# Optimization experiments

Measured on AMD Instinct MI355X. Metric: run time of the kernel, lower is better.

## Reference

```python
import jax, jax.numpy as jnp
import numpy as np

N, E, D = 100000, 640000, 128


def _xavier(key, shape):
    return jax.random.normal(key, shape, jnp.float32) * np.float32(np.sqrt(2.0 / (shape[0] + shape[1])))


def setup_inputs() -> dict:
    key = jax.random.key(0)
    ks = jax.random.split(key, 16)
    inp = {
        "x": jax.random.normal(ks[0], (N, D), jnp.float32),
        "prompt_h": jax.random.normal(ks[1], (N, D), jnp.float32),
        "edge_attr": jax.random.normal(ks[2], (E, D), jnp.float32),
        "prompt_e": jax.random.normal(ks[3], (E, D), jnp.float32),
        "edge_index": jax.random.randint(ks[4], (2, E), 0, N, dtype=jnp.int32),
        # Linear weights stored [in, out] (torch stores [out, in]; math identical)
        "Wq": _xavier(ks[5], (D, D)), "bq": jnp.zeros((D,), jnp.float32),
        "Wk": _xavier(ks[6], (D, D)), "bk": jnp.zeros((D,), jnp.float32),
        "Wv": _xavier(ks[7], (D, D)), "bv": jnp.zeros((D,), jnp.float32),
        "We1": _xavier(ks[8], (D, D)), "be1": jnp.zeros((D,), jnp.float32),
        "We2": _xavier(ks[9], (D, D)), "be2": jnp.zeros((D,), jnp.float32),
        "Wh": _xavier(ks[10], (D, D)), "bh": jnp.zeros((D,), jnp.float32),
        "Wf1": _xavier(ks[11], (D, 2 * D)), "bf1": jnp.zeros((2 * D,), jnp.float32),
        "Wf2": _xavier(ks[12], (2 * D, D)), "bf2": jnp.zeros((D,), jnp.float32),
    }
    return inp


def reference(x, prompt_h, edge_attr, prompt_e, edge_index,
              Wq, bq, Wk, bk, Wv, bv, We1, be1, We2, be2,
              Wh, bh, Wf1, bf1, Wf2, bf2):
    relu = jax.nn.relu
    # Projections (dropout=0, eval mode)
    Q = x @ Wq + bq                      # [N, D]
    K = prompt_h @ Wk + bk               # [N, D]
    V = prompt_h @ Wv + bv               # [N, D]
    h = relu(Q * K)                      # attn_product='mul', score_act with relu
    # Edge-enhanced messages: gather source node scores per edge
    src = h[edge_index[0]]               # [E, D]
    e = relu((edge_attr + prompt_e) @ We1 + be1)
    e = relu((e + prompt_e) @ We2 + be2)  # updated edge_attr (update_e=True)
    msg = relu(src + e)                  # [E, D]
    # scatter-add aggregation into destination nodes
    aggr = jax.ops.segment_sum(msg, edge_index[1], num_segments=x.shape[0])  # [N, D]
    h_out = relu((h + V + aggr) @ Wh + bh)
    h_out = h_out + x                    # residual (in_dim == out_dim)
    h_out = relu(h_out @ Wf1 + bf1)
    h_out = h_out @ Wf2 + bf2            # [N, D]
    return h_out, e
```

## Files before the change

kernel.cpp:

```cpp
#include <hip/hip_runtime.h>

typedef __attribute__((ext_vector_type(8))) short bfrag;
typedef __attribute__((ext_vector_type(4))) float f4;

__device__ __forceinline__ unsigned short f2b(float f) {
  unsigned int u = __builtin_bit_cast(unsigned int, f);
  u = (u + 0x7fffu + ((u >> 16) & 1u)) >> 16;
  return (unsigned short)u;
}
__device__ __forceinline__ float b2f(unsigned short s) {
  unsigned int u = ((unsigned int)s) << 16;
  return __builtin_bit_cast(float, u);
}
__device__ __forceinline__ float relu(float v) { return v > 0.f ? v : 0.f; }

template <bool ADD>
__device__ __forceinline__ void stage_A(char* dst, const float* s0, const float* s1,
                                        long r0, long maxRow) {
  const int tid = threadIdx.x;
#pragma unroll
  for (int i = 0; i < 4; ++i) {
    int ch = tid + (i << 8);
    int row = ch >> 4, kg = ch & 15;
    long gr = r0 + row;
    float v[8];
    if (gr < maxRow) {
      const float4* p = (const float4*)(s0 + gr * 128 + kg * 8);
      float4 a = p[0], b = p[1];
      v[0] = a.x; v[1] = a.y; v[2] = a.z; v[3] = a.w;
      v[4] = b.x; v[5] = b.y; v[6] = b.z; v[7] = b.w;
      if (ADD) {
        const float4* q = (const float4*)(s1 + gr * 128 + kg * 8);
        float4 c = q[0], d = q[1];
        v[0] += c.x; v[1] += c.y; v[2] += c.z; v[3] += c.w;
        v[4] += d.x; v[5] += d.y; v[6] += d.z; v[7] += d.w;
      }
    } else {
#pragma unroll
      for (int j = 0; j < 8; ++j) v[j] = 0.f;
    }
    union { unsigned short h[8]; uint4 u; } pk;
#pragma unroll
    for (int j = 0; j < 8; ++j) pk.h[j] = f2b(v[j]);
    *(uint4*)(dst + (((row << 8) + (kg << 4)) ^ ((row & 7) << 4))) = pk.u;
  }
}

__device__ __forceinline__ void stage_W(char* dst, const unsigned short* src,
                                        int rowStride, int kOff) {
  const int tid = threadIdx.x;
#pragma unroll
  for (int i = 0; i < 8; ++i) {
    int ch = tid + (i << 8);
    int col = ch >> 4, kg = ch & 15;
    uint4 u = *(const uint4*)(src + (size_t)col * rowStride + kOff + kg * 8);
    *(uint4*)(dst + (((col << 8) + (kg << 4)) ^ ((col & 7) << 4))) = u;
  }
}

__device__ __forceinline__ void stage_Wh(char* dst, const unsigned short* src,
                                         int rowStride, int kOff) {
  const int tid = threadIdx.x;
#pragma unroll
  for (int i = 0; i < 4; ++i) {
    int ch = tid + (i << 8);
    int c = ch >> 3, kg = ch & 7;
    uint4 u = *(const uint4*)(src + (size_t)c * rowStride + kOff + kg * 8);
    *(uint4*)(dst + (((c << 7) + (kg << 4)) ^ ((c & 7) << 4))) = u;
  }
}

__device__ __forceinline__ void mm(const char* A, const char* W, int wm, int wn,
                                   int lane, f4 acc[2][4]) {
#pragma unroll
  for (int kk = 0; kk < 4; ++kk) {
    bfrag a[2], b[4];
#pragma unroll
    for (int rt = 0; rt < 2; ++rt) {
      int row = (wm << 5) + (rt << 4) + (lane & 15);
      a[rt] = *(const bfrag*)(A + (((row << 8) + (kk << 6) + ((lane >> 4) << 4)) ^ ((row & 7) << 4)));
    }
#pragma unroll
    for (int ct = 0; ct < 4; ++ct) {
      int col = (wn << 6) + (ct << 4) + (lane & 15);
      b[ct] = *(const bfrag*)(W + (((col << 8) + (kk << 6) + ((lane >> 4) << 4)) ^ ((col & 7) << 4)));
    }
#pragma unroll
    for (int rt = 0; rt < 2; ++rt)
#pragma unroll
      for (int ct = 0; ct < 4; ++ct)
        acc[rt][ct] = __builtin_amdgcn_mfma_f32_16x16x32_bf16(a[rt], b[ct], acc[rt][ct], 0, 0, 0);
  }
}

__device__ __forceinline__ void mm_h(const char* A, const char* W, int wm, int wn,
                                     int lane, f4 acc[2][4], int kh) {
#pragma unroll
  for (int kk2 = 0; kk2 < 2; ++kk2) {
    int kA = (kh << 1) + kk2;
    bfrag a[2], b[4];
#pragma unroll
    for (int rt = 0; rt < 2; ++rt) {
      int row = (wm << 5) + (rt << 4) + (lane & 15);
      a[rt] = *(const bfrag*)(A + (((row << 8) + (kA << 6) + ((lane >> 4) << 4)) ^ ((row & 7) << 4)));
    }
#pragma unroll
    for (int ct = 0; ct < 4; ++ct) {
      int col = (wn << 6) + (ct << 4) + (lane & 15);
      b[ct] = *(const bfrag*)(W + (((col << 7) + (kk2 << 6) + ((lane >> 4) << 4)) ^ ((col & 7) << 4)));
    }
#pragma unroll
    for (int rt = 0; rt < 2; ++rt)
#pragma unroll
      for (int ct = 0; ct < 4; ++ct)
        acc[rt][ct] = __builtin_amdgcn_mfma_f32_16x16x32_bf16(a[rt], b[ct], acc[rt][ct], 0, 0, 0);
  }
}

__global__ void k_prep(const float* __restrict__ Wq, const float* __restrict__ Wk,
                       const float* __restrict__ Wv, const float* __restrict__ We1,
                       const float* __restrict__ We2, const float* __restrict__ Wh,
                       const float* __restrict__ Wf1, const float* __restrict__ Wf2,
                       unsigned short* __restrict__ wt) {
  int b = blockIdx.x, t = threadIdx.x;
  if (b < 384) {
    int m = b >> 6;
    const float* tbl[6] = {Wq, Wk, Wv, We1, We2, Wh};
    const float* src = tbl[m];
    int local = ((b & 63) << 8) + t;
    int n = local >> 7, k = local & 127;
    wt[m * 16384 + local] = f2b(src[k * 128 + n]);
  } else if (b < 512) {
    int local = ((b - 384) << 8) + t;
    int n = local >> 7, k = local & 127;
    wt[98304 + local] = f2b(Wf1[k * 256 + n]);
  } else {
    int local = ((b - 512) << 8) + t;
    int n = local >> 8, k = local & 255;
    wt[131072 + local] = f2b(Wf2[k * 128 + n]);
  }
}

__global__ void k_deg(const int* __restrict__ ei, int* __restrict__ deg, long E) {
  long g = (long)blockIdx.x * 256 + threadIdx.x;
  if (g < E) atomicAdd(deg + ei[E + g], 1);
}

__global__ void k_scanA(const int* __restrict__ deg, int* __restrict__ ex,
                        int* __restrict__ bsum, int n) {
  __shared__ int s[256];
  int t = threadIdx.x; int g = blockIdx.x * 256 + t;
  int v = (g < n) ? deg[g] : 0;
  int val = v;
  s[t] = val; __syncthreads();
#pragma unroll
  for (int o = 1; o < 256; o <<= 1) {
    int u = (t >= o) ? s[t - o] : 0;
    __syncthreads();
    val += u; s[t] = val;
    __syncthreads();
  }
  if (g < n) ex[g] = val - v;
  if (t == 255) bsum[blockIdx.x] = val;
}

__global__ void k_scanB(int* __restrict__ bsum, int nb) {
  __shared__ int s[1024];
  int t = threadIdx.x;
  int v = (t < nb) ? bsum[t] : 0;
  int val = v;
  s[t] = val; __syncthreads();
#pragma unroll
  for (int o = 1; o < 1024; o <<= 1) {
    int u = (t >= o) ? s[t - o] : 0;
    __syncthreads();
    val += u; s[t] = val;
    __syncthreads();
  }
  if (t < nb) bsum[t] = val - v;
}

__global__ void k_scanC(const int* __restrict__ ex, const int* __restrict__ bsum,
                        int* __restrict__ off, int* __restrict__ cursor, int n) {
  int g = blockIdx.x * 256 + threadIdx.x;
  if (g < n) {
    int o = ex[g] + bsum[blockIdx.x];
    off[g] = o; cursor[g] = o;
  }
}

__global__ void k_fill(const int* __restrict__ ei, int* __restrict__ cursor,
                       int* __restrict__ eidx, long E) {
  long g = (long)blockIdx.x * 256 + threadIdx.x;
  if (g < E) {
    int pos = atomicAdd(cursor + ei[E + g], 1);
    eidx[pos] = (int)g;
  }
}

__global__ __launch_bounds__(256, 2) void k_nodes1(
    const float* __restrict__ x, const float* __restrict__ ph,
    const float* __restrict__ bq, const float* __restrict__ bk,
    const float* __restrict__ bv, const unsigned short* __restrict__ wt,
    unsigned short* __restrict__ hbf, float* __restrict__ hpv, long N) {
  extern __shared__ char sm[];
  char* Ax = sm;
  char* Aph = sm + 16384;
  char* Wl = sm + 32768;
  long n0 = (long)blockIdx.x * 64;
  stage_A<false>(Ax, x, nullptr, n0, N);
  stage_A<false>(Aph, ph, nullptr, n0, N);
  stage_W(Wl, wt + 0, 128, 0);
  __syncthreads();
  const int tid = threadIdx.x, lane = tid & 63, w = tid >> 6, wm = w >> 1, wn = w & 1;
  f4 accQ[2][4] = {};
  mm(Ax, Wl, wm, wn, lane, accQ);
  __syncthreads();
  stage_W(Wl, wt + 16384, 128, 0);
  __syncthreads();
  f4 accK[2][4] = {};
  mm(Aph, Wl, wm, wn, lane, accK);
  __syncthreads();
  stage_W(Wl, wt + 32768, 128, 0);
  __syncthreads();
  f4 accV[2][4] = {};
  mm(Aph, Wl, wm, wn, lane, accV);
#pragma unroll
  for (int ct = 0; ct < 4; ++ct) {
    int col = (wn << 6) + (ct << 4) + (lane & 15);
    float vbq = bq[col], vbk = bk[col], vbv = bv[col];
#pragma unroll
    for (int rt = 0; rt < 2; ++rt)
#pragma unroll
      for (int j = 0; j < 4; ++j) {
        int rl = (wm << 5) + (rt << 4) + ((lane >> 4) << 2) + j;
        long row = n0 + rl;
        if (row < N) {
          float q = accQ[rt][ct][j] + vbq;
          float k = accK[rt][ct][j] + vbk;
          float v = accV[rt][ct][j] + vbv;
          float h = relu(q * k);
          hbf[row * 128 + col] = f2b(h);
          hpv[row * 128 + col] = h + v;
        }
      }
  }
}

__global__ __launch_bounds__(256, 3) void k_edges(
    const float* __restrict__ ea, const float* __restrict__ pe,
    const float* __restrict__ be1, const float* __restrict__ be2,
    const unsigned short* __restrict__ wt, const int* __restrict__ ei,
    const unsigned short* __restrict__ hbf, unsigned short* __restrict__ msg,
    float* __restrict__ eout, long E) {
  extern __shared__ char sm[];
  char* A = sm;
  unsigned short* peL = (unsigned short*)(sm + 16384);
  char* Wl = sm + 32768;
  char* stg = sm + 16384;
  int* srcI = (int*)(sm + 49152);
  const int tid = threadIdx.x;
  long e0 = (long)blockIdx.x * 64;
  if (tid < 64) srcI[tid] = (e0 + tid < E) ? ei[e0 + tid] : 0;
#pragma unroll
  for (int i = 0; i < 4; ++i) {
    int ch = tid + (i << 8);
    int row = ch >> 4, kg = ch & 15;
    long gr = e0 + row;
    union { unsigned short h[8]; uint4 u; } s, q;
    if (gr < E) {
      const float4* pa = (const float4*)(ea + gr * 128 + kg * 8);
      const float4* pp = (const float4*)(pe + gr * 128 + kg * 8);
      float4 a0 = pa[0], a1 = pa[1];
      float4 p0 = pp[0], p1 = pp[1];
      s.h[0] = f2b(a0.x + p0.x); s.h[1] = f2b(a0.y + p0.y);
      s.h[2] = f2b(a0.z + p0.z); s.h[3] = f2b(a0.w + p0.w);
      s.h[4] = f2b(a1.x + p1.x); s.h[5] = f2b(a1.y + p1.y);
      s.h[6] = f2b(a1.z + p1.z); s.h[7] = f2b(a1.w + p1.w);
      q.h[0] = f2b(p0.x); q.h[1] = f2b(p0.y); q.h[2] = f2b(p0.z); q.h[3] = f2b(p0.w);
      q.h[4] = f2b(p1.x); q.h[5] = f2b(p1.y); q.h[6] = f2b(p1.z); q.h[7] = f2b(p1.w);
    } else {
      s.u = uint4{0, 0, 0, 0}; q.u = uint4{0, 0, 0, 0};
    }
    *(uint4*)((char*)peL + (row << 8) + (kg << 4)) = q.u;
    *(uint4*)(A + (((row << 8) + (kg << 4)) ^ ((row & 7) << 4))) = s.u;
  }
  stage_Wh(Wl, wt + 49152, 128, 0);
  __syncthreads();
  const int lane = tid & 63, w = tid >> 6, wm = w >> 1, wn = w & 1;
  f4 acc[2][4] = {};
  mm_h(A, Wl, wm, wn, lane, acc, 0);
  __syncthreads();
  stage_Wh(Wl, wt + 49152, 128, 64);
  __syncthreads();
  mm_h(A, Wl, wm, wn, lane, acc, 1);
  __syncthreads();
  const int c0 = (tid & 31) << 2;
  const float4 vb1 = *(const float4*)(be1 + c0);
#pragma unroll
  for (int h = 0; h < 2; ++h) {
    if (wm == h) {
#pragma unroll
      for (int ct = 0; ct < 4; ++ct) {
        int col = (wn << 6) + (ct << 4) + (lane & 15);
#pragma unroll
        for (int rt = 0; rt < 2; ++rt)
#pragma unroll
          for (int j = 0; j < 4; ++j) {
            int lr = (rt << 4) + ((lane >> 4) << 2) + j;
            *(float*)(Wl + (((lr << 9) + (col << 2)) ^ ((lr & 7) << 4))) = acc[rt][ct][j];
          }
      }
    }
    __syncthreads();
#pragma unroll
    for (int it = 0; it < 4; ++it) {
      int lr = (tid >> 5) + (it << 3);
      int r = (h << 5) + lr;
      f4 a = *(const f4*)(Wl + (((lr << 9) + (c0 << 2)) ^ ((lr & 7) << 4)));
      uint2 pu = *(const uint2*)(peL + (r << 7) + c0);
      float p0 = b2f((unsigned short)pu.x), p1 = b2f((unsigned short)(pu.x >> 16));
      float p2 = b2f((unsigned short)pu.y), p3 = b2f((unsigned short)(pu.y >> 16));
      unsigned short t0 = f2b(relu(a[0] + vb1.x) + p0);
      unsigned short t1 = f2b(relu(a[1] + vb1.y) + p1);
      unsigned short t2 = f2b(relu(a[2] + vb1.z) + p2);
      unsigned short t3 = f2b(relu(a[3] + vb1.w) + p3);
      uint2 op;
      op.x = (unsigned int)t0 | ((unsigned int)t1 << 16);
      op.y = (unsigned int)t2 | ((unsigned int)t3 << 16);
      *(uint2*)(A + (((r << 8) + (c0 << 1)) ^ ((r & 7) << 4))) = op;
    }
    __syncthreads();
  }
  stage_Wh(Wl, wt + 65536, 128, 0);
  __syncthreads();
  f4 acc2[2][4] = {};
  mm_h(A, Wl, wm, wn, lane, acc2, 0);
  __syncthreads();
  stage_Wh(Wl, wt + 65536, 128, 64);
  __syncthreads();
  mm_h(A, Wl, wm, wn, lane, acc2, 1);
  __syncthreads();
#pragma unroll
  for (int ct = 0; ct < 4; ++ct) {
    int col = (wn << 6) + (ct << 4) + (lane & 15);
#pragma unroll
    for (int rt = 0; rt < 2; ++rt)
#pragma unroll
      for (int j = 0; j < 4; ++j) {
        int rl = (wm << 5) + (rt << 4) + ((lane >> 4) << 2) + j;
        *(float*)(stg + (((rl << 9) + (col << 2)) ^ ((rl & 7) << 4))) = acc2[rt][ct][j];
      }
  }
  __syncthreads();
  const float4 vb2 = *(const float4*)(be2 + c0);
#pragma unroll
  for (int it = 0; it < 8; ++it) {
    int r = (tid >> 5) + (it << 3);
    long edge = e0 + r;
    if (edge < E) {
      f4 a = *(const f4*)(stg + (((r << 9) + (c0 << 2)) ^ ((r & 7) << 4)));
      float ev0 = relu(a[0] + vb2.x), ev1 = relu(a[1] + vb2.y);
      float ev2 = relu(a[2] + vb2.z), ev3 = relu(a[3] + vb2.w);
      float4 ov; ov.x = ev0; ov.y = ev1; ov.z = ev2; ov.w = ev3;
      *(float4*)(eout + edge * 128 + c0) = ov;
      uint2 hu = *(const uint2*)(hbf + (long)srcI[r] * 128 + c0);
      float h0 = b2f((unsigned short)hu.x), h1 = b2f((unsigned short)(hu.x >> 16));
      float h2 = b2f((unsigned short)hu.y), h3 = b2f((unsigned short)(hu.y >> 16));
      unsigned short m0 = f2b(relu(ev0 + h0)), m1 = f2b(relu(ev1 + h1));
      unsigned short m2 = f2b(relu(ev2 + h2)), m3 = f2b(relu(ev3 + h3));
      uint2 mo;
      mo.x = (unsigned int)m0 | ((unsigned int)m1 << 16);
      mo.y = (unsigned int)m2 | ((unsigned int)m3 << 16);
      *(uint2*)(msg + edge * 128 + c0) = mo;
    }
  }
}

__global__ __launch_bounds__(256, 2) void k_edges_at(
    const float* __restrict__ ea, const float* __restrict__ pe,
    const float* __restrict__ be1, const float* __restrict__ be2,
    const unsigned short* __restrict__ wt, const int* __restrict__ ei,
    const unsigned short* __restrict__ hbf, float* __restrict__ aggr,
    float* __restrict__ eout, long E) {
  extern __shared__ char sm[];
  char* A = sm;
  unsigned short* peL = (unsigned short*)(sm + 16384);
  char* Wl = sm + 32768;
  int* srcI = (int*)(sm + 65536);
  int* dstI = srcI + 64;
  const int tid = threadIdx.x;
  long e0 = (long)blockIdx.x * 64;
  if (tid < 64) {
    long ge = e0 + tid;
    srcI[tid] = (ge < E) ? ei[ge] : 0;
    dstI[tid] = (ge < E) ? ei[E + ge] : 0;
  }
#pragma unroll
  for (int i = 0; i < 4; ++i) {
    int ch = tid + (i << 8);
    int row = ch >> 4, kg = ch & 15;
    long gr = e0 + row;
    union { unsigned short h[8]; uint4 u; } s, q;
    if (gr < E) {
      const float4* pa = (const float4*)(ea + gr * 128 + kg * 8);
      const float4* pp = (const float4*)(pe + gr * 128 + kg * 8);
      float4 a0 = pa[0], a1 = pa[1];
      float4 p0 = pp[0], p1 = pp[1];
      s.h[0] = f2b(a0.x + p0.x); s.h[1] = f2b(a0.y + p0.y);
      s.h[2] = f2b(a0.z + p0.z); s.h[3] = f2b(a0.w + p0.w);
      s.h[4] = f2b(a1.x + p1.x); s.h[5] = f2b(a1.y + p1.y);
      s.h[6] = f2b(a1.z + p1.z); s.h[7] = f2b(a1.w + p1.w);
      q.h[0] = f2b(p0.x); q.h[1] = f2b(p0.y); q.h[2] = f2b(p0.z); q.h[3] = f2b(p0.w);
      q.h[4] = f2b(p1.x); q.h[5] = f2b(p1.y); q.h[6] = f2b(p1.z); q.h[7] = f2b(p1.w);
    } else {
      s.u = uint4{0, 0, 0, 0}; q.u = uint4{0, 0, 0, 0};
    }
    *(uint4*)((char*)peL + (row << 8) + (kg << 4)) = q.u;
    *(uint4*)(A + (((row << 8) + (kg << 4)) ^ ((row & 7) << 4))) = s.u;
  }
  stage_W(Wl, wt + 49152, 128, 0);
  __syncthreads();
  const int lane = tid & 63, w = tid >> 6, wm = w >> 1, wn = w & 1;
  f4 acc[2][4] = {};
  mm(A, Wl, wm, wn, lane, acc);
  __syncthreads();
#pragma unroll
  for (int ct = 0; ct < 4; ++ct) {
    int col = (wn << 6) + (ct << 4) + (lane & 15);
    float b1 = be1[col];
#pragma unroll
    for (int rt = 0; rt < 2; ++rt)
#pragma unroll
      for (int j = 0; j < 4; ++j) {
        int rl = (wm << 5) + (rt << 4) + ((lane >> 4) << 2) + j;
        float tv = relu(acc[rt][ct][j] + b1) + b2f(peL[rl * 128 + col]);
        *(unsigned short*)(A + (((rl << 8) + (col << 1)) ^ ((rl & 7) << 4))) = f2b(tv);
      }
  }
  stage_W(Wl, wt + 65536, 128, 0);
  __syncthreads();
  f4 acc2[2][4] = {};
  mm(A, Wl, wm, wn, lane, acc2);
#pragma unroll
  for (int ct = 0; ct < 4; ++ct) {
    int col = (wn << 6) + (ct << 4) + (lane & 15);
    float b2 = be2[col];
#pragma unroll
    for (int rt = 0; rt < 2; ++rt)
#pragma unroll
      for (int j = 0; j < 4; ++j) {
        int rl = (wm << 5) + (rt << 4) + ((lane >> 4) << 2) + j;
        long edge = e0 + rl;
        if (edge < E) {
          float ev = relu(acc2[rt][ct][j] + b2);
          eout[edge * 128 + col] = ev;
          float hs = b2f(hbf[(long)srcI[rl] * 128 + col]);
          float m = relu(ev + hs);
          atomicAdd(aggr + (long)dstI[rl] * 128 + col, m);
        }
      }
  }
}

__global__ __launch_bounds__(256) void k_aggr(
    const int* __restrict__ off, const int* __restrict__ deg,
    const int* __restrict__ eidx, const unsigned short* __restrict__ msg,
    float* __restrict__ aggr, long N) {
  long node = (long)blockIdx.x * 4 + (threadIdx.x >> 6);
  if (node >= N) return;
  const int lane = threadIdx.x & 63;
  int st = off[node], d = deg[node];
  float a0 = 0.f, a1 = 0.f;
  for (int i = 0; i < d; ++i) {
    int eid = eidx[st + i];
    unsigned int u = *(const unsigned int*)(msg + (long)eid * 128 + lane * 2);
    a0 += b2f((unsigned short)u);
    a1 += b2f((unsigned short)(u >> 16));
  }
  *(float2*)(aggr + node * 128 + lane * 2) = float2{a0, a1};
}

__global__ __launch_bounds__(256, 2) void k_nodes2(
    const float* __restrict__ hpv, const float* __restrict__ aggr,
    const float* __restrict__ x, const float* __restrict__ bh,
    const float* __restrict__ bf1, const float* __restrict__ bf2,
    const unsigned short* __restrict__ wt, float* __restrict__ out, long N) {
  extern __shared__ char sm[];
  char* A = sm;
  char* T = sm + 16384;
  char* Wl = sm + 32768;
  long n0 = (long)blockIdx.x * 64;
  const int tid = threadIdx.x;
  stage_A<true>(A, hpv, aggr, n0, N);
  stage_W(Wl, wt + 81920, 128, 0);
  __syncthreads();
  const int lane = tid & 63, w = tid >> 6, wm = w >> 1, wn = w & 1;
  f4 acc1[2][4] = {};
  mm(A, Wl, wm, wn, lane, acc1);
  __syncthreads();
#pragma unroll
  for (int ct = 0; ct < 4; ++ct) {
    int col = (wn << 6) + (ct << 4) + (lane & 15);
    float bb = bh[col];
#pragma unroll
    for (int rt = 0; rt < 2; ++rt)
#pragma unroll
      for (int j = 0; j < 4; ++j) {
        int rl = (wm << 5) + (rt << 4) + ((lane >> 4) << 2) + j;
        long row = n0 + rl;
        float xv = (row < N) ? x[row * 128 + col] : 0.f;
        float tv = relu(acc1[rt][ct][j] + bb) + xv;
        *(unsigned short*)(T + (((rl << 8) + (col << 1)) ^ ((rl & 7) << 4))) = f2b(tv);
      }
  }
  stage_W(Wl, wt + 98304, 128, 0);
  __syncthreads();
  f4 accA[2][4] = {};
  mm(T, Wl, wm, wn, lane, accA);
  __syncthreads();
#pragma unroll
  for (int ct = 0; ct < 4; ++ct) {
    int col = (wn << 6) + (ct << 4) + (lane & 15);
    float bb = bf1[col];
#pragma unroll
    for (int rt = 0; rt < 2; ++rt)
#pragma unroll
      for (int j = 0; j < 4; ++j) {
        int rl = (wm << 5) + (rt << 4) + ((lane >> 4) << 2) + j;
        float uv = relu(accA[rt][ct][j] + bb);
        *(unsigned short*)(A + (((rl << 8) + (col << 1)) ^ ((rl & 7) << 4))) = f2b(uv);
      }
  }
  stage_W(Wl, wt + 131072, 256, 0);
  __syncthreads();
  f4 acc3[2][4] = {};
  mm(A, Wl, wm, wn, lane, acc3);
  __syncthreads();
  stage_W(Wl, wt + 114688, 128, 0);
  __syncthreads();
  f4 accB[2][4] = {};
  mm(T, Wl, wm, wn, lane, accB);
  __syncthreads();
#pragma unroll
  for (int ct = 0; ct < 4; ++ct) {
    int col = (wn << 6) + (ct << 4) + (lane & 15);
    float bb = bf1[128 + col];
#pragma unroll
    for (int rt = 0; rt < 2; ++rt)
#pragma unroll
      for (int j = 0; j < 4; ++j) {
        int rl = (wm << 5) + (rt << 4) + ((lane >> 4) << 2) + j;
        float uv = relu(accB[rt][ct][j] + bb);
        *(unsigned short*)(A + (((rl << 8) + (col << 1)) ^ ((rl & 7) << 4))) = f2b(uv);
      }
  }
  stage_W(Wl, wt + 131072, 256, 128);
  __syncthreads();
  mm(A, Wl, wm, wn, lane, acc3);
#pragma unroll
  for (int ct = 0; ct < 4; ++ct) {
    int col = (wn << 6) + (ct << 4) + (lane & 15);
    float bb = bf2[col];
#pragma unroll
    for (int rt = 0; rt < 2; ++rt)
#pragma unroll
      for (int j = 0; j < 4; ++j) {
        int rl = (wm << 5) + (rt << 4) + ((lane >> 4) << 2) + j;
        long row = n0 + rl;
        if (row < N) out[row * 128 + col] = acc3[rt][ct][j] + bb;
      }
  }
}

extern "C" void kernel_launch(void* const* d_in, const int* in_sizes, int n_in,
                              void* d_out, int out_size, void* d_ws, size_t ws_size,
                              hipStream_t stream) {
  const float* x   = (const float*)d_in[0];
  const float* ph  = (const float*)d_in[1];
  const float* ea  = (const float*)d_in[2];
  const float* pe  = (const float*)d_in[3];
  const int*   ei  = (const int*)d_in[4];
  const float* Wq  = (const float*)d_in[5];  const float* bq  = (const float*)d_in[6];
  const float* Wk  = (const float*)d_in[7];  const float* bk  = (const float*)d_in[8];
  const float* Wv  = (const float*)d_in[9];  const float* bv  = (const float*)d_in[10];
  const float* We1 = (const float*)d_in[11]; const float* be1 = (const float*)d_in[12];
  const float* We2 = (const float*)d_in[13]; const float* be2 = (const float*)d_in[14];
  const float* Wh  = (const float*)d_in[15]; const float* bh  = (const float*)d_in[16];
  const float* Wf1 = (const float*)d_in[17]; const float* bf1 = (const float*)d_in[18];
  const float* Wf2 = (const float*)d_in[19]; const float* bf2 = (const float*)d_in[20];
  const long N = in_sizes[0] / 128;
  const long E = in_sizes[2] / 128;

  char* ws = (char*)d_ws;
  size_t pos = 0;
  auto alloc = [&](size_t bytes) { size_t p = pos; pos += (bytes + 255) & ~255ULL; return p; };
  size_t o_wt   = alloc(327680);
  size_t o_hbf  = alloc((size_t)N * 256);
  size_t o_hpv  = alloc((size_t)N * 512);
  size_t o_aggr = alloc((size_t)N * 512);
  size_t base_needed = pos;
  size_t o_deg  = alloc((size_t)N * 4);
  size_t o_ex   = alloc((size_t)N * 4);
  size_t o_cur  = alloc((size_t)N * 4);
  size_t o_off  = alloc((size_t)N * 4);
  size_t o_bsum = alloc(4096);
  size_t o_eidx = alloc((size_t)E * 4);
  size_t o_msg  = alloc((size_t)E * 256);
  size_t csr_needed = pos;
  (void)base_needed;

  unsigned short* wt  = (unsigned short*)(ws + o_wt);
  unsigned short* hbf = (unsigned short*)(ws + o_hbf);
  float* hpv  = (float*)(ws + o_hpv);
  float* aggr = (float*)(ws + o_aggr);
  float* outH = (float*)d_out;
  float* outE = outH + N * 128;

  k_prep<<<640, 256, 0, stream>>>(Wq, Wk, Wv, We1, We2, Wh, Wf1, Wf2, wt);
  int nb = (int)((N + 63) / 64);
  int eb = (int)((E + 63) / 64);
  k_nodes1<<<nb, 256, 65536, stream>>>(x, ph, bq, bk, bv, wt, hbf, hpv, N);

  if (ws_size >= csr_needed) {
    int* deg = (int*)(ws + o_deg);
    int* ex  = (int*)(ws + o_ex);
    int* cur = (int*)(ws + o_cur);
    int* off = (int*)(ws + o_off);
    int* bsum = (int*)(ws + o_bsum);
    int* eidx = (int*)(ws + o_eidx);
    unsigned short* msg = (unsigned short*)(ws + o_msg);
    int nb1 = (int)((N + 255) / 256);
    hipMemsetAsync(deg, 0, (size_t)N * 4, stream);
    k_deg<<<(int)((E + 255) / 256), 256, 0, stream>>>(ei, deg, E);
    k_scanA<<<nb1, 256, 0, stream>>>(deg, ex, bsum, (int)N);
    k_scanB<<<1, 1024, 0, stream>>>(bsum, nb1);
    k_scanC<<<nb1, 256, 0, stream>>>(ex, bsum, off, cur, (int)N);
    k_fill<<<(int)((E + 255) / 256), 256, 0, stream>>>(ei, cur, eidx, E);
    k_edges<<<eb, 256, 49408, stream>>>(ea, pe, be1, be2, wt, ei, hbf, msg, outE, E);
    k_aggr<<<(int)((N + 3) / 4), 256, 0, stream>>>(off, deg, eidx, msg, aggr, N);
  } else {
    hipMemsetAsync(aggr, 0, (size_t)N * 512, stream);
    k_edges_at<<<eb, 256, 66048, stream>>>(ea, pe, be1, be2, wt, ei, hbf, aggr, outE, E);
  }
  k_nodes2<<<nb, 256, 65536, stream>>>(hpv, aggr, x, bh, bf1, bf2, wt, outH, N);
}
```

Before: 624.4 us.

## Write messages in CSR order and fuse aggregation into node MLP kernel

k_fill now records each edge's destination slot, and k_edges writes its message directly at that CSR position, so aggregation reads contiguous rows instead of following an index array. The separate k_aggr kernel and the fp32 aggr buffer round trip are removed: k_nodes2 gathers its segment sums straight into its shared-memory A tile. Shared-memory footprints are cut (half-width weight staging, one A buffer, edge-side data held in registers) and launch bounds raised to fit more blocks per CU, and node outputs go out as coalesced row stores through an LDS staging tile. The risks are higher register pressure from the per-thread arrays and extra barriers from the split weight staging.

```diff
diff --git a/kernel.cpp b/kernel.cpp
--- a/kernel.cpp
+++ b/kernel.cpp
@@ -114,6 +114,60 @@
 #pragma unroll
       for (int ct = 0; ct < 4; ++ct)
         acc[rt][ct] = __builtin_amdgcn_mfma_f32_16x16x32_bf16(a[rt], b[ct], acc[rt][ct], 0, 0, 0);
+  }
+}
+
+__device__ __forceinline__ void dump_half(char* Wl, const f4 acc[2][4], int lane, int wn) {
+#pragma unroll
+  for (int ct = 0; ct < 4; ++ct) {
+    int col = (wn << 6) + (ct << 4) + (lane & 15);
+#pragma unroll
+    for (int rt = 0; rt < 2; ++rt)
+#pragma unroll
+      for (int j = 0; j < 4; ++j) {
+        int lr = (rt << 4) + ((lane >> 4) << 2) + j;
+        *(float*)(Wl + (((lr << 9) + (col << 2)) ^ ((lr & 7) << 4))) = acc[rt][ct][j];
+      }
+  }
+}
+
+__device__ __forceinline__ void dump_full(char* stg, const f4 acc[2][4], int lane, int wm, int wn) {
+#pragma unroll
+  for (int ct = 0; ct < 4; ++ct) {
+    int col = (wn << 6) + (ct << 4) + (lane & 15);
+#pragma unroll
+    for (int rt = 0; rt < 2; ++rt)
+#pragma unroll
+      for (int j = 0; j < 4; ++j) {
+        int rl = (wm << 5) + (rt << 4) + ((lane >> 4) << 2) + j;
+        *(float*)(stg + (((rl << 9) + (col << 2)) ^ ((rl & 7) << 4))) = acc[rt][ct][j];
+      }
+  }
+}
+
+template <bool ADDX>
+__device__ __forceinline__ void trans_half(const char* Wl, char* dstT, const float* xsrc,
+                                           float4 vb, long n0, long N,
+                                           int h, int team, int c0) {
+#pragma unroll
+  for (int it = 0; it < 4; ++it) {
+    int lr = team + (it << 3);
+    int r = (h << 5) + lr;
+    f4 a = *(const f4*)(Wl + (((lr << 9) + (c0 << 2)) ^ ((lr & 7) << 4)));
+    float x0 = 0.f, x1 = 0.f, x2 = 0.f, x3 = 0.f;
+    long row = n0 + r;
+    if (ADDX && row < N) {
+      float4 xv = *(const float4*)(xsrc + row * 128 + c0);
+      x0 = xv.x; x1 = xv.y; x2 = xv.z; x3 = xv.w;
+    }
+    float t0 = relu(a[0] + vb.x) + x0;
+    float t1 = relu(a[1] + vb.y) + x1;
+    float t2 = relu(a[2] + vb.z) + x2;
+    float t3 = relu(a[3] + vb.w) + x3;
+    uint2 op;
+    op.x = (unsigned)f2b(t0) | ((unsigned)f2b(t1) << 16);
+    op.y = (unsigned)f2b(t2) | ((unsigned)f2b(t3) << 16);
+    *(uint2*)(dstT + (((r << 8) + (c0 << 1)) ^ ((r & 7) << 4))) = op;
   }
 }
 
@@ -190,41 +244,39 @@
 }
 
 __global__ void k_fill(const int* __restrict__ ei, int* __restrict__ cursor,
-                       int* __restrict__ eidx, long E) {
+                       int* __restrict__ pos, long E) {
   long g = (long)blockIdx.x * 256 + threadIdx.x;
-  if (g < E) {
-    int pos = atomicAdd(cursor + ei[E + g], 1);
-    eidx[pos] = (int)g;
-  }
-}
-
-__global__ __launch_bounds__(256, 2) void k_nodes1(
+  if (g < E) pos[g] = atomicAdd(cursor + ei[E + g], 1);
+}
+
+__global__ __launch_bounds__(256, 3) void k_nodes1(
     const float* __restrict__ x, const float* __restrict__ ph,
     const float* __restrict__ bq, const float* __restrict__ bk,
     const float* __restrict__ bv, const unsigned short* __restrict__ wt,
     unsigned short* __restrict__ hbf, float* __restrict__ hpv, long N) {
   extern __shared__ char sm[];
-  char* Ax = sm;
-  char* Aph = sm + 16384;
-  char* Wl = sm + 32768;
+  char* A = sm;
+  char* Wl = sm + 16384;
   long n0 = (long)blockIdx.x * 64;
-  stage_A<false>(Ax, x, nullptr, n0, N);
-  stage_A<false>(Aph, ph, nullptr, n0, N);
+  const int tid = threadIdx.x, lane = tid & 63, w = tid >> 6, wm = w >> 1, wn = w & 1;
+  const int team = tid >> 5, c0 = (tid & 31) << 2;
+  stage_A<false>(A, x, nullptr, n0, N);
   stage_W(Wl, wt + 0, 128, 0);
   __syncthreads();
-  const int tid = threadIdx.x, lane = tid & 63, w = tid >> 6, wm = w >> 1, wn = w & 1;
   f4 accQ[2][4] = {};
-  mm(Ax, Wl, wm, wn, lane, accQ);
-  __syncthreads();
+  mm(A, Wl, wm, wn, lane, accQ);
+  __syncthreads();
+  stage_A<false>(A, ph, nullptr, n0, N);
   stage_W(Wl, wt + 16384, 128, 0);
   __syncthreads();
   f4 accK[2][4] = {};
-  mm(Aph, Wl, wm, wn, lane, accK);
+  mm(A, Wl, wm, wn, lane, accK);
   __syncthreads();
   stage_W(Wl, wt + 32768, 128, 0);
   __syncthreads();
   f4 accV[2][4] = {};
-  mm(Aph, Wl, wm, wn, lane, accV);
+  mm(A, Wl, wm, wn, lane, accV);
+  __syncthreads();
 #pragma unroll
   for (int ct = 0; ct < 4; ++ct) {
     int col = (wn << 6) + (ct << 4) + (lane & 15);
@@ -234,34 +286,149 @@
 #pragma unroll
       for (int j = 0; j < 4; ++j) {
         int rl = (wm << 5) + (rt << 4) + ((lane >> 4) << 2) + j;
-        long row = n0 + rl;
-        if (row < N) {
-          float q = accQ[rt][ct][j] + vbq;
-          float k = accK[rt][ct][j] + vbk;
-          float v = accV[rt][ct][j] + vbv;
-          float h = relu(q * k);
-          hbf[row * 128 + col] = f2b(h);
-          hpv[row * 128 + col] = h + v;
-        }
+        float q = accQ[rt][ct][j] + vbq;
+        float k = accK[rt][ct][j] + vbk;
+        float v = accV[rt][ct][j] + vbv;
+        float h = relu(q * k);
+        *(unsigned short*)(A + (((rl << 8) + (col << 1)) ^ ((rl & 7) << 4))) = f2b(h);
+        *(float*)(Wl + (((rl << 9) + (col << 2)) ^ ((rl & 7) << 4))) = h + v;
       }
   }
-}
-
-__global__ __launch_bounds__(256, 3) void k_edges(
+  __syncthreads();
+#pragma unroll
+  for (int it = 0; it < 8; ++it) {
+    int r = team + (it << 3);
+    long row = n0 + r;
+    if (row < N) {
+      uint2 hb = *(const uint2*)(A + (((r << 8) + (c0 << 1)) ^ ((r & 7) << 4)));
+      f4 hv = *(const f4*)(Wl + (((r << 9) + (c0 << 2)) ^ ((r & 7) << 4)));
+      *(uint2*)(hbf + row * 128 + c0) = hb;
+      float4 ov; ov.x = hv[0]; ov.y = hv[1]; ov.z = hv[2]; ov.w = hv[3];
+      *(float4*)(hpv + row * 128 + c0) = ov;
+    }
+  }
+}
+
+__global__ __launch_bounds__(256, 5) void k_edges(
     const float* __restrict__ ea, const float* __restrict__ pe,
     const float* __restrict__ be1, const float* __restrict__ be2,
     const unsigned short* __restrict__ wt, const int* __restrict__ ei,
-    const unsigned short* __restrict__ hbf, unsigned short* __restrict__ msg,
+    const int* __restrict__ pos, const unsigned short* __restrict__ hbf,
+    unsigned short* __restrict__ msg, float* __restrict__ eout, long E) {
+  extern __shared__ char sm[];
+  char* A = sm;
+  char* Wl = sm + 16384;
+  char* stg = sm;
+  const int tid = threadIdx.x;
+  const int team = tid >> 5, c0 = (tid & 31) << 2;
+  const int lane = tid & 63, w = tid >> 6, wm = w >> 1, wn = w & 1;
+  long e0 = (long)blockIdx.x * 64;
+
+  int srcR[8], posR[8];
+  uint2 peR[8];
+#pragma unroll
+  for (int it = 0; it < 8; ++it) {
+    int r = team + (it << 3);
+    long ge = e0 + r;
+    srcR[it] = (ge < E) ? ei[ge] : 0;
+    posR[it] = (ge < E) ? pos[ge] : 0;
+    float4 av = make_float4(0.f, 0.f, 0.f, 0.f), pv = av;
+    if (ge < E) {
+      av = *(const float4*)(ea + ge * 128 + c0);
+      pv = *(const float4*)(pe + ge * 128 + c0);
+    }
+    peR[it].x = (unsigned)f2b(pv.x) | ((unsigned)f2b(pv.y) << 16);
+    peR[it].y = (unsigned)f2b(pv.z) | ((unsigned)f2b(pv.w) << 16);
+    uint2 s;
+    s.x = (unsigned)f2b(av.x + pv.x) | ((unsigned)f2b(av.y + pv.y) << 16);
+    s.y = (unsigned)f2b(av.z + pv.z) | ((unsigned)f2b(av.w + pv.w) << 16);
+    *(uint2*)(A + (((r << 8) + (c0 << 1)) ^ ((r & 7) << 4))) = s;
+  }
+  stage_Wh(Wl, wt + 49152, 128, 0);
+  __syncthreads();
+  f4 acc[2][4] = {};
+  mm_h(A, Wl, wm, wn, lane, acc, 0);
+  __syncthreads();
+  stage_Wh(Wl, wt + 49152, 128, 64);
+  __syncthreads();
+  mm_h(A, Wl, wm, wn, lane, acc, 1);
+  __syncthreads();
+  const float4 vb1 = *(const float4*)(be1 + c0);
+#pragma unroll
+  for (int h = 0; h < 2; ++h) {
+    if (wm == h) dump_half(Wl, acc, lane, wn);
+    __syncthreads();
+#pragma unroll
+    for (int it = 0; it < 4; ++it) {
+      int lr = team + (it << 3);
+      int r = (h << 5) + lr;
+      int j = (h << 2) + it;
+      f4 a = *(const f4*)(Wl + (((lr << 9) + (c0 << 2)) ^ ((lr & 7) << 4)));
+      float p0 = b2f((unsigned short)peR[j].x), p1 = b2f((unsigned short)(peR[j].x >> 16));
+      float p2 = b2f((unsigned short)peR[j].y), p3 = b2f((unsigned short)(peR[j].y >> 16));
+      float t0 = relu(a[0] + vb1.x) + p0;
+      float t1 = relu(a[1] + vb1.y) + p1;
+      float t2 = relu(a[2] + vb1.z) + p2;
+      float t3 = relu(a[3] + vb1.w) + p3;
+      uint2 op;
+      op.x = (unsigned)f2b(t0) | ((unsigned)f2b(t1) << 16);
+      op.y = (unsigned)f2b(t2) | ((unsigned)f2b(t3) << 16);
+      *(uint2*)(A + (((r << 8) + (c0 << 1)) ^ ((r & 7) << 4))) = op;
+    }
+    __syncthreads();
+  }
+  stage_Wh(Wl, wt + 65536, 128, 0);
+  __syncthreads();
+  f4 acc2[2][4] = {};
+  mm_h(A, Wl, wm, wn, lane, acc2, 0);
+  __syncthreads();
+  stage_Wh(Wl, wt + 65536, 128, 64);
+  __syncthreads();
+  mm_h(A, Wl, wm, wn, lane, acc2, 1);
+  __syncthreads();
+  dump_full(stg, acc2, lane, wm, wn);
+  __syncthreads();
+  const float4 vb2 = *(const float4*)(be2 + c0);
+#pragma unroll
+  for (int it = 0; it < 8; ++it) {
+    int r = team + (it << 3);
+    long edge = e0 + r;
+    if (edge < E) {
+      f4 a = *(const f4*)(stg + (((r << 9) + (c0 << 2)) ^ ((r & 7) << 4)));
+      float ev0 = relu(a[0] + vb2.x), ev1 = relu(a[1] + vb2.y);
+      float ev2 = relu(a[2] + vb2.z), ev3 = relu(a[3] + vb2.w);
+      float4 ov; ov.x = ev0; ov.y = ev1; ov.z = ev2; ov.w = ev3;
+      *(float4*)(eout + edge * 128 + c0) = ov;
+      uint2 hu = *(const uint2*)(hbf + (long)srcR[it] * 128 + c0);
+      float h0 = b2f((unsigned short)hu.x), h1 = b2f((unsigned short)(hu.x >> 16));
+      float h2 = b2f((unsigned short)hu.y), h3 = b2f((unsigned short)(hu.y >> 16));
+      uint2 mo;
+      mo.x = (unsigned)f2b(relu(ev0 + h0)) | ((unsigned)f2b(relu(ev1 + h1)) << 16);
+      mo.y = (unsigned)f2b(relu(ev2 + h2)) | ((unsigned)f2b(relu(ev3 + h3)) << 16);
+      *(uint2*)(msg + (long)posR[it] * 128 + c0) = mo;
+    }
+  }
+}
+
+__global__ __launch_bounds__(256, 2) void k_edges_at(
+    const float* __restrict__ ea, const float* __restrict__ pe,
+    const float* __restrict__ be1, const float* __restrict__ be2,
+    const unsigned short* __restrict__ wt, const int* __restrict__ ei,
+    const unsigned short* __restrict__ hbf, float* __restrict__ aggr,
     float* __restrict__ eout, long E) {
   extern __shared__ char sm[];
   char* A = sm;
   unsigned short* peL = (unsigned short*)(sm + 16384);
   char* Wl = sm + 32768;
-  char* stg = sm + 16384;
-  int* srcI = (int*)(sm + 49152);
+  int* srcI = (int*)(sm + 65536);
+  int* dstI = srcI + 64;
   const int tid = threadIdx.x;
   long e0 = (long)blockIdx.x * 64;
-  if (tid < 64) srcI[tid] = (e0 + tid < E) ? ei[e0 + tid] : 0;
+  if (tid < 64) {
+    long ge = e0 + tid;
+    srcI[tid] = (ge < E) ? ei[ge] : 0;
+    dstI[tid] = (ge < E) ? ei[E + ge] : 0;
+  }
 #pragma unroll
   for (int i = 0; i < 4; ++i) {
     int ch = tid + (i << 8);
@@ -285,140 +452,6 @@
     *(uint4*)((char*)peL + (row << 8) + (kg << 4)) = q.u;
     *(uint4*)(A + (((row << 8) + (kg << 4)) ^ ((row & 7) << 4))) = s.u;
   }
-  stage_Wh(Wl, wt + 49152, 128, 0);
-  __syncthreads();
-  const int lane = tid & 63, w = tid >> 6, wm = w >> 1, wn = w & 1;
-  f4 acc[2][4] = {};
-  mm_h(A, Wl, wm, wn, lane, acc, 0);
-  __syncthreads();
-  stage_Wh(Wl, wt + 49152, 128, 64);
-  __syncthreads();
-  mm_h(A, Wl, wm, wn, lane, acc, 1);
-  __syncthreads();
-  const int c0 = (tid & 31) << 2;
-  const float4 vb1 = *(const float4*)(be1 + c0);
-#pragma unroll
-  for (int h = 0; h < 2; ++h) {
-    if (wm == h) {
-#pragma unroll
-      for (int ct = 0; ct < 4; ++ct) {
-        int col = (wn << 6) + (ct << 4) + (lane & 15);
-#pragma unroll
-        for (int rt = 0; rt < 2; ++rt)
-#pragma unroll
-          for (int j = 0; j < 4; ++j) {
-            int lr = (rt << 4) + ((lane >> 4) << 2) + j;
-            *(float*)(Wl + (((lr << 9) + (col << 2)) ^ ((lr & 7) << 4))) = acc[rt][ct][j];
-          }
-      }
-    }
-    __syncthreads();
-#pragma unroll
-    for (int it = 0; it < 4; ++it) {
-      int lr = (tid >> 5) + (it << 3);
-      int r = (h << 5) + lr;
-      f4 a = *(const f4*)(Wl + (((lr << 9) + (c0 << 2)) ^ ((lr & 7) << 4)));
-      uint2 pu = *(const uint2*)(peL + (r << 7) + c0);
-      float p0 = b2f((unsigned short)pu.x), p1 = b2f((unsigned short)(pu.x >> 16));
-      float p2 = b2f((unsigned short)pu.y), p3 = b2f((unsigned short)(pu.y >> 16));
-      unsigned short t0 = f2b(relu(a[0] + vb1.x) + p0);
-      unsigned short t1 = f2b(relu(a[1] + vb1.y) + p1);
-      unsigned short t2 = f2b(relu(a[2] + vb1.z) + p2);
-      unsigned short t3 = f2b(relu(a[3] + vb1.w) + p3);
-      uint2 op;
-      op.x = (unsigned int)t0 | ((unsigned int)t1 << 16);
-      op.y = (unsigned int)t2 | ((unsigned int)t3 << 16);
-      *(uint2*)(A + (((r << 8) + (c0 << 1)) ^ ((r & 7) << 4))) = op;
-    }
-    __syncthreads();
-  }
-  stage_Wh(Wl, wt + 65536, 128, 0);
-  __syncthreads();
-  f4 acc2[2][4] = {};
-  mm_h(A, Wl, wm, wn, lane, acc2, 0);
-  __syncthreads();
-  stage_Wh(Wl, wt + 65536, 128, 64);
-  __syncthreads();
-  mm_h(A, Wl, wm, wn, lane, acc2, 1);
-  __syncthreads();
-#pragma unroll
-  for (int ct = 0; ct < 4; ++ct) {
-    int col = (wn << 6) + (ct << 4) + (lane & 15);
-#pragma unroll
-    for (int rt = 0; rt < 2; ++rt)
-#pragma unroll
-      for (int j = 0; j < 4; ++j) {
-        int rl = (wm << 5) + (rt << 4) + ((lane >> 4) << 2) + j;
-        *(float*)(stg + (((rl << 9) + (col << 2)) ^ ((rl & 7) << 4))) = acc2[rt][ct][j];
-      }
-  }
-  __syncthreads();
-  const float4 vb2 = *(const float4*)(be2 + c0);
-#pragma unroll
-  for (int it = 0; it < 8; ++it) {
-    int r = (tid >> 5) + (it << 3);
-    long edge = e0 + r;
-    if (edge < E) {
-      f4 a = *(const f4*)(stg + (((r << 9) + (c0 << 2)) ^ ((r & 7) << 4)));
-      float ev0 = relu(a[0] + vb2.x), ev1 = relu(a[1] + vb2.y);
-      float ev2 = relu(a[2] + vb2.z), ev3 = relu(a[3] + vb2.w);
-      float4 ov; ov.x = ev0; ov.y = ev1; ov.z = ev2; ov.w = ev3;
-      *(float4*)(eout + edge * 128 + c0) = ov;
-      uint2 hu = *(const uint2*)(hbf + (long)srcI[r] * 128 + c0);
-      float h0 = b2f((unsigned short)hu.x), h1 = b2f((unsigned short)(hu.x >> 16));
-      float h2 = b2f((unsigned short)hu.y), h3 = b2f((unsigned short)(hu.y >> 16));
-      unsigned short m0 = f2b(relu(ev0 + h0)), m1 = f2b(relu(ev1 + h1));
-      unsigned short m2 = f2b(relu(ev2 + h2)), m3 = f2b(relu(ev3 + h3));
-      uint2 mo;
-      mo.x = (unsigned int)m0 | ((unsigned int)m1 << 16);
-      mo.y = (unsigned int)m2 | ((unsigned int)m3 << 16);
-      *(uint2*)(msg + edge * 128 + c0) = mo;
-    }
-  }
-}
-
-__global__ __launch_bounds__(256, 2) void k_edges_at(
-    const float* __restrict__ ea, const float* __restrict__ pe,
-    const float* __restrict__ be1, const float* __restrict__ be2,
-    const unsigned short* __restrict__ wt, const int* __restrict__ ei,
-    const unsigned short* __restrict__ hbf, float* __restrict__ aggr,
-    float* __restrict__ eout, long E) {
-  extern __shared__ char sm[];
-  char* A = sm;
-  unsigned short* peL = (unsigned short*)(sm + 16384);
-  char* Wl = sm + 32768;
-  int* srcI = (int*)(sm + 65536);
-  int* dstI = srcI + 64;
-  const int tid = threadIdx.x;
-  long e0 = (long)blockIdx.x * 64;
-  if (tid < 64) {
-    long ge = e0 + tid;
-    srcI[tid] = (ge < E) ? ei[ge] : 0;
-    dstI[tid] = (ge < E) ? ei[E + ge] : 0;
-  }
-#pragma unroll
-  for (int i = 0; i < 4; ++i) {
-    int ch = tid + (i << 8);
-    int row = ch >> 4, kg = ch & 15;
-    long gr = e0 + row;
-    union { unsigned short h[8]; uint4 u; } s, q;
-    if (gr < E) {
-      const float4* pa = (const float4*)(ea + gr * 128 + kg * 8);
-      const float4* pp = (const float4*)(pe + gr * 128 + kg * 8);
-      float4 a0 = pa[0], a1 = pa[1];
-      float4 p0 = pp[0], p1 = pp[1];
-      s.h[0] = f2b(a0.x + p0.x); s.h[1] = f2b(a0.y + p0.y);
-      s.h[2] = f2b(a0.z + p0.z); s.h[3] = f2b(a0.w + p0.w);
-      s.h[4] = f2b(a1.x + p1.x); s.h[5] = f2b(a1.y + p1.y);
-      s.h[6] = f2b(a1.z + p1.z); s.h[7] = f2b(a1.w + p1.w);
-      q.h[0] = f2b(p0.x); q.h[1] = f2b(p0.y); q.h[2] = f2b(p0.z); q.h[3] = f2b(p0.w);
-      q.h[4] = f2b(p1.x); q.h[5] = f2b(p1.y); q.h[6] = f2b(p1.z); q.h[7] = f2b(p1.w);
-    } else {
-      s.u = uint4{0, 0, 0, 0}; q.u = uint4{0, 0, 0, 0};
-    }
-    *(uint4*)((char*)peL + (row << 8) + (kg << 4)) = q.u;
-    *(uint4*)(A + (((row << 8) + (kg << 4)) ^ ((row & 7) << 4))) = s.u;
-  }
   stage_W(Wl, wt + 49152, 128, 0);
   __syncthreads();
   const int lane = tid & 63, w = tid >> 6, wm = w >> 1, wn = w & 1;
@@ -463,26 +496,11 @@
   }
 }
 
-__global__ __launch_bounds__(256) void k_aggr(
+template <bool GATHER>
+__global__ __launch_bounds__(256, 3) void k_nodes2(
+    const float* __restrict__ hpv, const float* __restrict__ aggr,
     const int* __restrict__ off, const int* __restrict__ deg,
-    const int* __restrict__ eidx, const unsigned short* __restrict__ msg,
-    float* __restrict__ aggr, long N) {
-  long node = (long)blockIdx.x * 4 + (threadIdx.x >> 6);
-  if (node >= N) return;
-  const int lane = threadIdx.x & 63;
-  int st = off[node], d = deg[node];
-  float a0 = 0.f, a1 = 0.f;
-  for (int i = 0; i < d; ++i) {
-    int eid = eidx[st + i];
-    unsigned int u = *(const unsigned int*)(msg + (long)eid * 128 + lane * 2);
-    a0 += b2f((unsigned short)u);
-    a1 += b2f((unsigned short)(u >> 16));
-  }
-  *(float2*)(aggr + node * 128 + lane * 2) = float2{a0, a1};
-}
-
-__global__ __launch_bounds__(256, 2) void k_nodes2(
-    const float* __restrict__ hpv, const float* __restrict__ aggr,
+    const unsigned short* __restrict__ msg,
     const float* __restrict__ x, const float* __restrict__ bh,
     const float* __restrict__ bf1, const float* __restrict__ bf2,
     const unsigned short* __restrict__ wt, float* __restrict__ out, long N) {
@@ -490,86 +508,131 @@
   char* A = sm;
   char* T = sm + 16384;
   char* Wl = sm + 32768;
+  char* stg = sm;
   long n0 = (long)blockIdx.x * 64;
   const int tid = threadIdx.x;
-  stage_A<true>(A, hpv, aggr, n0, N);
-  stage_W(Wl, wt + 81920, 128, 0);
-  __syncthreads();
+  const int team = tid >> 5, c0 = (tid & 31) << 2;
   const int lane = tid & 63, w = tid >> 6, wm = w >> 1, wn = w & 1;
+
+  if (GATHER) {
+#pragma unroll
+    for (int it = 0; it < 8; ++it) {
+      int r = team + (it << 3);
+      long node = n0 + r;
+      float s0 = 0.f, s1 = 0.f, s2 = 0.f, s3 = 0.f;
+      if (node < N) {
+        float4 hv = *(const float4*)(hpv + node * 128 + c0);
+        s0 = hv.x; s1 = hv.y; s2 = hv.z; s3 = hv.w;
+        int o = off[node], d = deg[node];
+        const unsigned short* mrow = msg + (long)o * 128 + c0;
+        int i = 0;
+        for (; i + 1 < d; i += 2) {
+          uint2 m0 = *(const uint2*)(mrow);
+          uint2 m1 = *(const uint2*)(mrow + 128);
+          mrow += 256;
+          s0 += b2f((unsigned short)m0.x) + b2f((unsigned short)m1.x);
+          s1 += b2f((unsigned short)(m0.x >> 16)) + b2f((unsigned short)(m1.x >> 16));
+          s2 += b2f((unsigned short)m0.y) + b2f((unsigned short)m1.y);
+          s3 += b2f((unsigned short)(m0.y >> 16)) + b2f((unsigned short)(m1.y >> 16));
+        }
+        if (i < d) {
+          uint2 m0 = *(const uint2*)(mrow);
+          s0 += b2f((unsigned short)m0.x);
+          s1 += b2f((unsigned short)(m0.x >> 16));
+          s2 += b2f((unsigned short)m0.y);
+          s3 += b2f((unsigned short)(m0.y >> 16));
+        }
+      }
+      uint2 pk;
+      pk.x = (unsigned)f2b(s0) | ((unsigned)f2b(s1) << 16);
+      pk.y = (unsigned)f2b(s2) | ((unsigned)f2b(s3) << 16);
+      *(uint2*)(A + (((r << 8) + (c0 << 1)) ^ ((r & 7) << 4))) = pk;
+    }
+  } else {
+    stage_A<true>(A, hpv, aggr, n0, N);
+  }
+  stage_Wh(Wl, wt + 81920, 128, 0);
+  __syncthreads();
   f4 acc1[2][4] = {};
-  mm(A, Wl, wm, wn, lane, acc1);
-  __syncthreads();
-#pragma unroll
-  for (int ct = 0; ct < 4; ++ct) {
-    int col = (wn << 6) + (ct << 4) + (lane & 15);
-    float bb = bh[col];
-#pragma unroll
-    for (int rt = 0; rt < 2; ++rt)
-#pragma unroll
-      for (int j = 0; j < 4; ++j) {
-        int rl = (wm << 5) + (rt << 4) + ((lane >> 4) << 2) + j;
-        long row = n0 + rl;
-        float xv = (row < N) ? x[row * 128 + col] : 0.f;
-        float tv = relu(acc1[rt][ct][j] + bb) + xv;
-        *(unsigned short*)(T + (((rl << 8) + (col << 1)) ^ ((rl & 7) << 4))) = f2b(tv);
-      }
-  }
-  stage_W(Wl, wt + 98304, 128, 0);
+  mm_h(A, Wl, wm, wn, lane, acc1, 0);
+  __syncthreads();
+  stage_Wh(Wl, wt + 81920, 128, 64);
+  __syncthreads();
+  mm_h(A, Wl, wm, wn, lane, acc1, 1);
+  __syncthreads();
+  float4 vbh = *(const float4*)(bh + c0);
+#pragma unroll
+  for (int h = 0; h < 2; ++h) {
+    if (wm == h) dump_half(Wl, acc1, lane, wn);
+    __syncthreads();
+    trans_half<true>(Wl, T, x, vbh, n0, N, h, team, c0);
+    __syncthreads();
+  }
+  stage_Wh(Wl, wt + 98304, 128, 0);
   __syncthreads();
   f4 accA[2][4] = {};
-  mm(T, Wl, wm, wn, lane, accA);
-  __syncthreads();
-#pragma unroll
-  for (int ct = 0; ct < 4; ++ct) {
-    int col = (wn << 6) + (ct << 4) + (lane & 15);
-    float bb = bf1[col];
-#pragma unroll
-    for (int rt = 0; rt < 2; ++rt)
-#pragma unroll
-      for (int j = 0; j < 4; ++j) {
-        int rl = (wm << 5) + (rt << 4) + ((lane >> 4) << 2) + j;
-        float uv = relu(accA[rt][ct][j] + bb);
-        *(unsigned short*)(A + (((rl << 8) + (col << 1)) ^ ((rl & 7) << 4))) = f2b(uv);
-      }
-  }
-  stage_W(Wl, wt + 131072, 256, 0);
+  mm_h(T, Wl, wm, wn, lane, accA, 0);
+  __syncthreads();
+  stage_Wh(Wl, wt + 98304, 128, 64);
+  __syncthreads();
+  mm_h(T, Wl, wm, wn, lane, accA, 1);
+  __syncthreads();
+  float4 vb1a = *(const float4*)(bf1 + c0);
+#pragma unroll
+  for (int h = 0; h < 2; ++h) {
+    if (wm == h) dump_half(Wl, accA, lane, wn);
+    __syncthreads();
+    trans_half<false>(Wl, A, nullptr, vb1a, n0, N, h, team, c0);
+    __syncthreads();
+  }
+  stage_Wh(Wl, wt + 131072, 256, 0);
   __syncthreads();
   f4 acc3[2][4] = {};
-  mm(A, Wl, wm, wn, lane, acc3);
-  __syncthreads();
-  stage_W(Wl, wt + 114688, 128, 0);
+  mm_h(A, Wl, wm, wn, lane, acc3, 0);
+  __syncthreads();
+  stage_Wh(Wl, wt + 131072, 256, 64);
+  __syncthreads();
+  mm_h(A, Wl, wm, wn, lane, acc3, 1);
+  __syncthreads();
+  stage_Wh(Wl, wt + 114688, 128, 0);
   __syncthreads();
   f4 accB[2][4] = {};
-  mm(T, Wl, wm, wn, lane, accB);
-  __syncthreads();
-#pragma unroll
-  for (int ct = 0; ct < 4; ++ct) {
-    int col = (wn << 6) + (ct << 4) + (lane & 15);
-    float bb = bf1[128 + col];
-#pragma unroll
-    for (int rt = 0; rt < 2; ++rt)
-#pragma unroll
-      for (int j = 0; j < 4; ++j) {
-        int rl = (wm << 5) + (rt << 4) + ((lane >> 4) << 2) + j;
-        float uv = relu(accB[rt][ct][j] + bb);
-        *(unsigned short*)(A + (((rl << 8) + (col << 1)) ^ ((rl & 7) << 4))) = f2b(uv);
-      }
-  }
-  stage_W(Wl, wt + 131072, 256, 128);
-  __syncthreads();
-  mm(A, Wl, wm, wn, lane, acc3);
-#pragma unroll
-  for (int ct = 0; ct < 4; ++ct) {
-    int col = (wn << 6) + (ct << 4) + (lane & 15);
-    float bb = bf2[col];
-#pragma unroll
-    for (int rt = 0; rt < 2; ++rt)
-#pragma unroll
-      for (int j = 0; j < 4; ++j) {
-        int rl = (wm << 5) + (rt << 4) + ((lane >> 4) << 2) + j;
-        long row = n0 + rl;
-        if (row < N) out[row * 128 + col] = acc3[rt][ct][j] + bb;
-      }
+  mm_h(T, Wl, wm, wn, lane, accB, 0);
+  __syncthreads();
+  stage_Wh(Wl, wt + 114688, 128, 64);
+  __syncthreads();
+  mm_h(T, Wl, wm, wn, lane, accB, 1);
+  __syncthreads();
+  float4 vb1b = *(const float4*)(bf1 + 128 + c0);
+#pragma unroll
+  for (int h = 0; h < 2; ++h) {
+    if (wm == h) dump_half(Wl, accB, lane, wn);
+    __syncthreads();
+    trans_half<false>(Wl, A, nullptr, vb1b, n0, N, h, team, c0);
+    __syncthreads();
+  }
+  stage_Wh(Wl, wt + 131072, 256, 128);
+  __syncthreads();
+  mm_h(A, Wl, wm, wn, lane, acc3, 0);
+  __syncthreads();
+  stage_Wh(Wl, wt + 131072, 256, 192);
+  __syncthreads();
+  mm_h(A, Wl, wm, wn, lane, acc3, 1);
+  __syncthreads();
+  dump_full(stg, acc3, lane, wm, wn);
+  __syncthreads();
+  float4 vb2 = *(const float4*)(bf2 + c0);
+#pragma unroll
+  for (int it = 0; it < 8; ++it) {
+    int r = team + (it << 3);
+    long row = n0 + r;
+    if (row < N) {
+      f4 a = *(const f4*)(stg + (((r << 9) + (c0 << 2)) ^ ((r & 7) << 4)));
+      float4 ov;
+      ov.x = a[0] + vb2.x; ov.y = a[1] + vb2.y;
+      ov.z = a[2] + vb2.z; ov.w = a[3] + vb2.w;
+      *(float4*)(out + row * 128 + c0) = ov;
+    }
   }
 }
 
@@ -593,22 +656,20 @@
   const long E = in_sizes[2] / 128;
 
   char* ws = (char*)d_ws;
-  size_t pos = 0;
-  auto alloc = [&](size_t bytes) { size_t p = pos; pos += (bytes + 255) & ~255ULL; return p; };
+  size_t pos_ = 0;
+  auto alloc = [&](size_t bytes) { size_t p = pos_; pos_ += (bytes + 255) & ~255ULL; return p; };
   size_t o_wt   = alloc(327680);
   size_t o_hbf  = alloc((size_t)N * 256);
   size_t o_hpv  = alloc((size_t)N * 512);
   size_t o_aggr = alloc((size_t)N * 512);
-  size_t base_needed = pos;
   size_t o_deg  = alloc((size_t)N * 4);
   size_t o_ex   = alloc((size_t)N * 4);
   size_t o_cur  = alloc((size_t)N * 4);
   size_t o_off  = alloc((size_t)N * 4);
   size_t o_bsum = alloc(4096);
-  size_t o_eidx = alloc((size_t)E * 4);
+  size_t o_pos  = alloc((size_t)E * 4);
   size_t o_msg  = alloc((size_t)E * 256);
-  size_t csr_needed = pos;
-  (void)base_needed;
+  size_t csr_needed = pos_;
 
   unsigned short* wt  = (unsigned short*)(ws + o_wt);
   unsigned short* hbf = (unsigned short*)(ws + o_hbf);
@@ -620,7 +681,7 @@
   k_prep<<<640, 256, 0, stream>>>(Wq, Wk, Wv, We1, We2, Wh, Wf1, Wf2, wt);
   int nb = (int)((N + 63) / 64);
   int eb = (int)((E + 63) / 64);
-  k_nodes1<<<nb, 256, 65536, stream>>>(x, ph, bq, bk, bv, wt, hbf, hpv, N);
+  k_nodes1<<<nb, 256, 49152, stream>>>(x, ph, bq, bk, bv, wt, hbf, hpv, N);
 
   if (ws_size >= csr_needed) {
     int* deg = (int*)(ws + o_deg);
@@ -628,7 +689,7 @@
     int* cur = (int*)(ws + o_cur);
     int* off = (int*)(ws + o_off);
     int* bsum = (int*)(ws + o_bsum);
-    int* eidx = (int*)(ws + o_eidx);
+    int* posA = (int*)(ws + o_pos);
     unsigned short* msg = (unsigned short*)(ws + o_msg);
     int nb1 = (int)((N + 255) / 256);
     hipMemsetAsync(deg, 0, (size_t)N * 4, stream);
@@ -636,12 +697,12 @@
     k_scanA<<<nb1, 256, 0, stream>>>(deg, ex, bsum, (int)N);
     k_scanB<<<1, 1024, 0, stream>>>(bsum, nb1);
     k_scanC<<<nb1, 256, 0, stream>>>(ex, bsum, off, cur, (int)N);
-    k_fill<<<(int)((E + 255) / 256), 256, 0, stream>>>(ei, cur, eidx, E);
-    k_edges<<<eb, 256, 49408, stream>>>(ea, pe, be1, be2, wt, ei, hbf, msg, outE, E);
-    k_aggr<<<(int)((N + 3) / 4), 256, 0, stream>>>(off, deg, eidx, msg, aggr, N);
+    k_fill<<<(int)((E + 255) / 256), 256, 0, stream>>>(ei, cur, posA, E);
+    k_edges<<<eb, 256, 32768, stream>>>(ea, pe, be1, be2, wt, ei, posA, hbf, msg, outE, E);
+    k_nodes2<true><<<nb, 256, 49152, stream>>>(hpv, nullptr, off, deg, msg, x, bh, bf1, bf2, wt, outH, N);
   } else {
     hipMemsetAsync(aggr, 0, (size_t)N * 512, stream);
     k_edges_at<<<eb, 256, 66048, stream>>>(ea, pe, be1, be2, wt, ei, hbf, aggr, outE, E);
-  }
-  k_nodes2<<<nb, 256, 65536, stream>>>(hpv, aggr, x, bh, bf1, bf2, wt, outH, N);
-}
+    k_nodes2<false><<<nb, 256, 49152, stream>>>(hpv, aggr, nullptr, nullptr, nullptr, x, bh, bf1, bf2, wt, outH, N);
+  }
+}
```

Result: slower. 1.223 ms (+95.9%).
